# Kernel optimization log

Hardware: AMD Instinct MI355X
Metric: run time of the kernel (lower is better)

Reference implementation:

```python
import jax, jax.numpy as jnp
import numpy as np

N, E, D, H, HID = 50000, 400000, 64, 8, 1024
NEG_SLOPE = 0.2
BN_EPS = 1e-5


def setup_inputs() -> dict:
    key = jax.random.key(0)
    ks = jax.random.split(key, 10)
    s = 0.05
    return {
        "x": jax.random.normal(ks[0], (N, D), jnp.float32),
        "src": jax.random.randint(ks[1], (E,), 0, N, jnp.int32),
        "dst": jax.random.randint(ks[2], (E,), 0, N, jnp.int32),
        "fc_w": jax.random.normal(ks[3], (H * D, D), jnp.float32) * s,
        "attn_l": jax.random.normal(ks[4], (H, D), jnp.float32) * s,
        "attn_r": jax.random.normal(ks[5], (H, D), jnp.float32) * s,
        "gat_bias": jnp.zeros((H * D,), jnp.float32),
        "bn1_gamma": jnp.ones((H * D,), jnp.float32),
        "bn1_beta": jnp.zeros((H * D,), jnp.float32),
        "w1": jax.random.normal(ks[6], (HID, H * D), jnp.float32) * s,
        "b1": jnp.zeros((HID,), jnp.float32),
        "w2": jax.random.normal(ks[7], (D, HID), jnp.float32) * s,
        "b2": jnp.zeros((D,), jnp.float32),
        "bn2_gamma": jnp.ones((D,), jnp.float32),
        "bn2_beta": jnp.zeros((D,), jnp.float32),
    }


def _batchnorm(h, gamma, beta):
    # training-mode BatchNorm1d: batch statistics over node axis
    mu = h.mean(axis=0)
    var = h.var(axis=0)
    return gamma * (h - mu) * jax.lax.rsqrt(var + BN_EPS) + beta


def reference(x, src, dst, fc_w, attn_l, attn_r, gat_bias,
              bn1_gamma, bn1_beta, w1, b1, w2, b2, bn2_gamma, bn2_beta):
    n = x.shape[0]
    nh, dh = attn_l.shape
    # --- GATConv ---
    feat = (x @ fc_w.T).reshape(n, nh, dh)                 # [N,H,Dh]
    el = jnp.einsum("nhd,hd->nh", feat, attn_l)            # [N,H]
    er = jnp.einsum("nhd,hd->nh", feat, attn_r)            # [N,H]
    e = jax.nn.leaky_relu(el[src] + er[dst], NEG_SLOPE)    # [E,H]
    # edge softmax grouped by destination node (numerically stable)
    emax = jax.ops.segment_max(e, dst, num_segments=n)
    emax = jnp.where(jnp.isfinite(emax), emax, 0.0)        # nodes w/ no in-edges
    ez = jnp.exp(e - emax[dst])
    denom = jax.ops.segment_sum(ez, dst, num_segments=n)
    alpha = ez / denom[dst]                                # [E,H]
    msg = alpha[:, :, None] * feat[src]                    # [E,H,Dh]
    rst = jax.ops.segment_sum(msg, dst, num_segments=n)    # [N,H,Dh]
    rst = rst + gat_bias.reshape(nh, dh)
    h = rst.reshape(n, nh * dh)                            # flatten(1)
    # --- feed forward: BN -> Linear -> ReLU -> Linear -> BN ---
    h = _batchnorm(h, bn1_gamma, bn1_beta)
    h = jax.nn.relu(h @ w1.T + b1)
    h = h @ w2.T + b2
    h = _batchnorm(h, bn2_gamma, bn2_beta)
    return h
```

## Files before the change

kernel.cpp:

```cpp
#include <hip/hip_runtime.h>

#define NEG_SLOPE 0.2f
#define BN_EPS 1e-5f

typedef __bf16 bf16x8 __attribute__((ext_vector_type(8)));
typedef float  f32x4  __attribute__((ext_vector_type(4)));
typedef unsigned short ushort8_t __attribute__((ext_vector_type(8)));

__device__ __forceinline__ unsigned short f2bf(float f) {
    unsigned int u = __float_as_uint(f);
    unsigned int r = u + 0x7FFFu + ((u >> 16) & 1u);
    return (unsigned short)(r >> 16);
}
__device__ __forceinline__ float bf2f(unsigned short u) {
    return __uint_as_float(((unsigned int)u) << 16);
}
__device__ __forceinline__ void gload16(const void* g, void* l) {
    __builtin_amdgcn_global_load_lds(
        (const __attribute__((address_space(1))) unsigned int*)g,
        (__attribute__((address_space(3))) unsigned int*)l, 16, 0, 0);
}

__global__ __launch_bounds__(256)
void prep(const float* __restrict__ x, const int* __restrict__ dst,
          const float* __restrict__ fc_w, const float* __restrict__ w2,
          const float* __restrict__ attn_l, const float* __restrict__ attn_r,
          unsigned short* __restrict__ xbf, unsigned short* __restrict__ fcwbf,
          unsigned short* __restrict__ w2bf, float* __restrict__ proj,
          int* __restrict__ counts, int totX4, int E,
          int bCvtx, int bHist, int bFcw, int bW2)
{
    const int bid = blockIdx.x, tid = threadIdx.x;
    if (bid < bCvtx) {
        int i4 = bid * 256 + tid;
        if (i4 < totX4) {
            float4 v = *(const float4*)(x + (size_t)i4 * 4);
            ushort4 o = {f2bf(v.x), f2bf(v.y), f2bf(v.z), f2bf(v.w)};
            *(ushort4*)(xbf + (size_t)i4 * 4) = o;
        }
    } else if (bid < bHist) {
        int base = (bid - bCvtx) * 1024 + tid;
        #pragma unroll
        for (int k = 0; k < 4; ++k) {
            int e = base + k * 256;
            if (e < E) atomicAdd(&counts[dst[e]], 1);
        }
    } else if (bid < bFcw) {
        int i4 = (bid - bHist) * 256 + tid;
        if (i4 < 8192) {
            float4 v = *(const float4*)(fc_w + (size_t)i4 * 4);
            ushort4 o = {f2bf(v.x), f2bf(v.y), f2bf(v.z), f2bf(v.w)};
            *(ushort4*)(fcwbf + (size_t)i4 * 4) = o;
        }
    } else if (bid < bW2) {
        int i4 = (bid - bFcw) * 256 + tid;
        if (i4 < 16384) {
            float4 v = *(const float4*)(w2 + (size_t)i4 * 4);
            ushort4 o = {f2bf(v.x), f2bf(v.y), f2bf(v.z), f2bf(v.w)};
            *(ushort4*)(w2bf + (size_t)i4 * 4) = o;
        }
    } else {
        for (int t2 = tid; t2 < 512; t2 += 256) {
            int h = t2 >> 6, k = t2 & 63;
            float al = 0.f, ar = 0.f;
            for (int d = 0; d < 64; ++d) {
                float w = fc_w[(size_t)(h * 64 + d) * 64 + k];
                al = fmaf(attn_l[h * 64 + d], w, al);
                ar = fmaf(attn_r[h * 64 + d], w, ar);
            }
            proj[t2] = al;
            proj[512 + t2] = ar;
        }
    }
}

__global__ __launch_bounds__(256)
void scan1_elr(const int* __restrict__ counts, int* __restrict__ incl,
               int* __restrict__ bsum, int N, int NB,
               const float* __restrict__ x, const float* __restrict__ proj,
               float* __restrict__ el, float* __restrict__ er, int NH)
{
    __shared__ int sm[256];
    if ((int)blockIdx.x < NB) {
        int i = blockIdx.x * 256 + threadIdx.x;
        int v = (i < N) ? counts[i] : 0;
        sm[threadIdx.x] = v;
        __syncthreads();
        #pragma unroll
        for (int d = 1; d < 256; d <<= 1) {
            int t = (threadIdx.x >= d) ? sm[threadIdx.x - d] : 0;
            __syncthreads();
            sm[threadIdx.x] += t;
            __syncthreads();
        }
        if (i < N) incl[i] = sm[threadIdx.x];
        if (threadIdx.x == 255) bsum[blockIdx.x] = sm[255];
    } else {
        int idx = (blockIdx.x - NB) * 256 + threadIdx.x;
        if (idx >= NH) return;
        int h = idx & 7, n = idx >> 3;
        const float4* f  = (const float4*)(x + (size_t)n * 64);
        const float4* pl = (const float4*)(proj + h * 64);
        const float4* pr = (const float4*)(proj + 512 + h * 64);
        float sl = 0.f, sr = 0.f;
        #pragma unroll
        for (int i = 0; i < 16; ++i) {
            float4 fv = f[i], lv = pl[i], rv = pr[i];
            sl += fv.x * lv.x + fv.y * lv.y + fv.z * lv.z + fv.w * lv.w;
            sr += fv.x * rv.x + fv.y * rv.y + fv.z * rv.z + fv.w * rv.w;
        }
        el[idx] = sl;
        er[idx] = sr;
    }
}

__global__ void scan2(int* __restrict__ bsum, int nb) {
    __shared__ int sm[256];
    int v = (threadIdx.x < nb) ? bsum[threadIdx.x] : 0;
    sm[threadIdx.x] = v;
    __syncthreads();
    #pragma unroll
    for (int d = 1; d < 256; d <<= 1) {
        int t = (threadIdx.x >= d) ? sm[threadIdx.x - d] : 0;
        __syncthreads();
        sm[threadIdx.x] += t;
        __syncthreads();
    }
    if (threadIdx.x < nb) bsum[threadIdx.x] = sm[threadIdx.x] - v;
}
__global__ void scan3(const int* __restrict__ incl, const int* __restrict__ bsum,
                      int* __restrict__ row_ptr, int* __restrict__ cursor, int N) {
    int i = blockIdx.x * 256 + threadIdx.x;
    if (i < N) {
        int v = incl[i] + bsum[blockIdx.x];
        row_ptr[i + 1] = v;
        cursor[i + 1] = v;
    }
    if (i == 0) { row_ptr[0] = 0; cursor[0] = 0; }
}
__global__ void scatter_edges(const int* __restrict__ src, const int* __restrict__ dst,
                              int* __restrict__ cursor, int* __restrict__ esrc, int E) {
    int e = blockIdx.x * 256 + threadIdx.x;
    if (e < E) {
        int p = atomicAdd(&cursor[dst[e]], 1);
        esrc[p] = src[e];
    }
}

__global__ __launch_bounds__(256)
void gat_aggregate(const int* __restrict__ row_ptr, const int* __restrict__ esrc,
                   const float* __restrict__ el, const float* __restrict__ er,
                   const unsigned short* __restrict__ xb, unsigned short* __restrict__ xagg,
                   int N)
{
    int node = blockIdx.x * 4 + (threadIdx.x >> 6);
    if (node >= N) return;
    const int lane = threadIdx.x & 63;
    const int h = lane >> 3, j = lane & 7;
    const int beg = row_ptr[node], end = row_ptr[node + 1];
    const float er_n = er[node * 8 + h];

    float denom = 0.f;
    float a[8] = {};
    for (int k = beg; k < end; ++k) {
        int s = esrc[k];
        float v = el[s * 8 + h] + er_n;
        v = (v > 0.f) ? v : NEG_SLOPE * v;
        float z = __expf(v);
        denom += z;
        ushort8_t fv = *(const ushort8_t*)(xb + (size_t)s * 64 + j * 8);
        #pragma unroll
        for (int t = 0; t < 8; ++t) a[t] = fmaf(z, bf2f(fv[t]), a[t]);
    }
    float inv = (end > beg) ? 1.f / denom : 0.f;
    ushort8_t o;
    #pragma unroll
    for (int t = 0; t < 8; ++t) o[t] = f2bf(a[t] * inv);
    *(ushort8_t*)(xagg + (size_t)node * 512 + lane * 8) = o;
}

__global__ __launch_bounds__(256)
void head_transform(const unsigned short* __restrict__ Xa,
                    const unsigned short* __restrict__ Fw,
                    const float* __restrict__ gat_bias,
                    unsigned short* __restrict__ H,
                    float* __restrict__ sums1, int M)
{
    __shared__ alignas(16) char Asm[128 * 64 * 2];
    __shared__ alignas(16) char Bsm[64 * 64 * 2];
    __shared__ float reds[4][64], redq[4][64];
    const int tid = threadIdx.x, lane = tid & 63, wave = tid >> 6;
    const int bm = blockIdx.x * 128;
    const int head = blockIdx.y;
    const int lr = lane >> 3, lk = ((lane & 7) ^ lr) * 8;

    #pragma unroll
    for (int it = 0; it < 4; ++it) {
        int seg = wave * 4 + it;
        gload16(Xa + (size_t)(bm + seg * 8 + lr) * 512 + head * 64 + lk, Asm + seg * 1024);
    }
    #pragma unroll
    for (int it = 0; it < 2; ++it) {
        int seg = wave * 2 + it;
        gload16(Fw + (size_t)(head * 64 + seg * 8 + lr) * 64 + lk, Bsm + seg * 1024);
    }
    __syncthreads();

    f32x4 acc[2][4] = {};
    #pragma unroll
    for (int kk = 0; kk < 2; ++kk) {
        int kg = kk * 4 + (lane >> 4);
        bf16x8 a[2], b[4];
        #pragma unroll
        for (int i = 0; i < 2; ++i) {
            int row = wave * 32 + i * 16 + (lane & 15);
            a[i] = *(const bf16x8*)(Asm + row * 128 + ((kg ^ (row & 7)) << 4));
        }
        #pragma unroll
        for (int j = 0; j < 4; ++j) {
            int row = j * 16 + (lane & 15);
            b[j] = *(const bf16x8*)(Bsm + row * 128 + ((kg ^ (row & 7)) << 4));
        }
        #pragma unroll
        for (int i = 0; i < 2; ++i)
            #pragma unroll
            for (int j = 0; j < 4; ++j)
                acc[i][j] = __builtin_amdgcn_mfma_f32_16x16x32_bf16(a[i], b[j], acc[i][j], 0, 0, 0);
    }

    float s4[4] = {}, q4[4] = {};
    #pragma unroll
    for (int j = 0; j < 4; ++j) {
        int col = j * 16 + (lane & 15);
        float bias = gat_bias[head * 64 + col];
        #pragma unroll
        for (int i = 0; i < 2; ++i)
            #pragma unroll
            for (int r = 0; r < 4; ++r) {
                int gm = bm + wave * 32 + i * 16 + (lane >> 4) * 4 + r;
                if (gm < M) {
                    unsigned short hb = f2bf(acc[i][j][r] + bias);
                    H[(size_t)gm * 512 + head * 64 + col] = hb;
                    float vq = bf2f(hb);
                    s4[j] += vq; q4[j] += vq * vq;
                }
            }
    }
    #pragma unroll
    for (int j = 0; j < 4; ++j) {
        s4[j] += __shfl_xor(s4[j], 16); q4[j] += __shfl_xor(q4[j], 16);
        s4[j] += __shfl_xor(s4[j], 32); q4[j] += __shfl_xor(q4[j], 32);
    }
    if (lane < 16) {
        #pragma unroll
        for (int j = 0; j < 4; ++j) {
            reds[wave][j * 16 + lane] = s4[j];
            redq[wave][j * 16 + lane] = q4[j];
        }
    }
    __syncthreads();
    if (wave == 0 && lane < 16) {
        #pragma unroll
        for (int j = 0; j < 4; ++j) {
            int c = j * 16 + lane;
            atomicAdd(&sums1[head * 64 + c], reds[0][c] + reds[1][c] + reds[2][c] + reds[3][c]);
            atomicAdd(&sums1[512 + head * 64 + c], redq[0][c] + redq[1][c] + redq[2][c] + redq[3][c]);
        }
    }
}

__global__ __launch_bounds__(256)
void fold_w1(const float* __restrict__ w1, const float* __restrict__ sums1,
             const float* __restrict__ gamma, const float* __restrict__ beta,
             const float* __restrict__ b1, unsigned short* __restrict__ w1p,
             float* __restrict__ b1p, float invM)
{
    __shared__ float sa[512], sb[512];
    for (int c = threadIdx.x; c < 512; c += 256) {
        float mu = sums1[c] * invM;
        float var = sums1[512 + c] * invM - mu * mu;
        float a = gamma[c] * rsqrtf(var + BN_EPS);
        sa[c] = a;
        sb[c] = beta[c] - a * mu;
    }
    __syncthreads();
    int n = blockIdx.x * 4 + (threadIdx.x >> 6);
    int lane = threadIdx.x & 63;
    const float* wrow = w1 + (size_t)n * 512 + lane * 8;
    float p = 0.f;
    ushort8_t o;
    #pragma unroll
    for (int t = 0; t < 8; ++t) {
        float w = wrow[t];
        o[t] = f2bf(w * sa[lane * 8 + t]);
        p = fmaf(w, sb[lane * 8 + t], p);
    }
    *(ushort8_t*)(w1p + (size_t)n * 512 + lane * 8) = o;
    #pragma unroll
    for (int d = 1; d < 64; d <<= 1) p += __shfl_xor(p, d);
    if (lane == 0) b1p[n] = b1[n] + p;
}

__global__ __launch_bounds__(256)
void gemm2p(const unsigned short* __restrict__ A,
            const unsigned short* __restrict__ B,
            const unsigned short* __restrict__ W2,
            const float* __restrict__ b1p,
            unsigned short* __restrict__ P, int M)
{
    __shared__ alignas(16) char smem[49152];
    char* Abuf0 = smem;
    char* Abuf1 = smem + 16384;
    char* Bbuf  = smem + 32768;
    char* TR   = smem;
    char* Wbuf = smem + 32768;
    char* PK   = smem + 32768;

    const int tid = threadIdx.x, lane = tid & 63, wave = tid >> 6;
    const int wr = wave >> 1, wc = wave & 1;
    const int lr = lane >> 3, lk = ((lane & 7) ^ lr) * 8;

    int bid = blockIdx.x;
    int wgid = (bid & 7) * 391 + (bid >> 3);
    const int bm = (wgid >> 3) * 128;
    const int t  = wgid & 7;
    const int bn = t * 128;

    #pragma unroll
    for (int it = 0; it < 4; ++it) {
        int seg = wave * 4 + it;
        gload16(A + (size_t)(bm + seg * 8 + lr) * 512 + lk, Abuf0 + seg * 1024);
    }

    f32x4 acc[4][4] = {};
    #pragma unroll
    for (int ks = 0; ks < 8; ++ks) {
        const int k0 = ks * 64;
        #pragma unroll
        for (int it = 0; it < 4; ++it) {
            int seg = wave * 4 + it;
            gload16(B + (size_t)(bn + seg * 8 + lr) * 512 + k0 + lk, Bbuf + seg * 1024);
        }
        if (ks < 7) {
            char* An = (ks & 1) ? Abuf0 : Abuf1;
            #pragma unroll
            for (int it = 0; it < 4; ++it) {
                int seg = wave * 4 + it;
                gload16(A + (size_t)(bm + seg * 8 + lr) * 512 + (k0 + 64) + lk, An + seg * 1024);
            }
            asm volatile("s_waitcnt vmcnt(4)" ::: "memory");
        } else {
            asm volatile("s_waitcnt vmcnt(0)" ::: "memory");
        }
        __builtin_amdgcn_s_barrier();
        __builtin_amdgcn_sched_barrier(0);
        const char* Ac = (ks & 1) ? Abuf1 : Abuf0;
        #pragma unroll
        for (int kk = 0; kk < 2; ++kk) {
            int kg = kk * 4 + (lane >> 4);
            bf16x8 a[4], b[4];
            #pragma unroll
            for (int i = 0; i < 4; ++i) {
                int row = wr * 64 + i * 16 + (lane & 15);
                a[i] = *(const bf16x8*)(Ac + row * 128 + ((kg ^ (row & 7)) << 4));
            }
            #pragma unroll
            for (int j = 0; j < 4; ++j) {
                int row = wc * 64 + j * 16 + (lane & 15);
                b[j] = *(const bf16x8*)(Bbuf + row * 128 + ((kg ^ (row & 7)) << 4));
            }
            #pragma unroll
            for (int i = 0; i < 4; ++i)
                #pragma unroll
                for (int j = 0; j < 4; ++j)
                    acc[i][j] = __builtin_amdgcn_mfma_f32_16x16x32_bf16(a[i], b[j], acc[i][j], 0, 0, 0);
        }
        __builtin_amdgcn_sched_barrier(0);
        __builtin_amdgcn_s_barrier();
        __builtin_amdgcn_sched_barrier(0);
    }

    #pragma unroll
    for (int j = 0; j < 4; ++j) {
        int c = wc * 64 + j * 16 + (lane & 15);
        float bs = b1p[bn + c];
        #pragma unroll
        for (int i = 0; i < 4; ++i)
            #pragma unroll
            for (int r = 0; r < 4; ++r) {
                int rw = wr * 64 + i * 16 + (lane >> 4) * 4 + r;
                float v = fmaxf(acc[i][j][r] + bs, 0.f);
                *(unsigned short*)(TR + rw * 256 + (((c >> 3) ^ (rw & 7)) << 4) + (c & 7) * 2) = f2bf(v);
            }
    }
    #pragma unroll
    for (int it = 0; it < 4; ++it) {
        int oc = wave * 16 + it * 4 + (lane >> 4);
        int g = lane & 15;
        gload16(W2 + (size_t)oc * 1024 + bn + ((g ^ (oc & 7))) * 8, Wbuf + (wave * 4 + it) * 1024);
    }
    __syncthreads();

    f32x4 pacc[2][4] = {};
    #pragma unroll
    for (int ks = 0; ks < 4; ++ks) {
        int kg2 = ks * 4 + (lane >> 4);
        #pragma unroll
        for (int i = 0; i < 2; ++i) {
            int arow = wave * 32 + i * 16 + (lane & 15);
            bf16x8 av = *(const bf16x8*)(TR + arow * 256 + ((kg2 ^ (arow & 7)) << 4));
            #pragma unroll
            for (int j = 0; j < 4; ++j) {
                int oc = j * 16 + (lane & 15);
                bf16x8 bv = *(const bf16x8*)(Wbuf + oc * 256 + ((kg2 ^ (oc & 7)) << 4));
                pacc[i][j] = __builtin_amdgcn_mfma_f32_16x16x32_bf16(av, bv, pacc[i][j], 0, 0, 0);
            }
        }
    }
    __syncthreads();

    #pragma unroll
    for (int i = 0; i < 2; ++i)
        #pragma unroll
        for (int j = 0; j < 4; ++j)
            #pragma unroll
            for (int r = 0; r < 4; ++r) {
                int row = wave * 32 + i * 16 + (lane >> 4) * 4 + r;
                int col = j * 16 + (lane & 15);
                *(unsigned short*)(PK + row * 128 + col * 2) = f2bf(pacc[i][j][r]);
            }
    __syncthreads();
    unsigned short* Pt = P + (size_t)t * M * 64;
    #pragma unroll
    for (int it = 0; it < 4; ++it) {
        int u = it * 256 + tid;
        int row = u >> 3, g8 = u & 7;
        int gm = bm + row;
        if (gm < M) {
            uint4 v = *(const uint4*)(PK + row * 128 + g8 * 16);
            *(uint4*)(Pt + (size_t)gm * 64 + g8 * 8) = v;
        }
    }
}

__global__ __launch_bounds__(256)
void reduce_bn2(const unsigned short* __restrict__ P, const float* __restrict__ b2,
                float* __restrict__ out, int M, float* __restrict__ sums2)
{
    __shared__ float ls[256], lq[256];
    int c = threadIdx.x & 63, g = threadIdx.x >> 6;
    const size_t S = (size_t)M * 64;
    float bias = b2[c];
    float s = 0.f, q = 0.f;
    for (int r = blockIdx.x * 4 + g; r < M; r += gridDim.x * 4) {
        size_t idx = (size_t)r * 64 + c;
        float v = bias;
        #pragma unroll
        for (int t = 0; t < 8; ++t) v += bf2f(P[t * S + idx]);
        out[idx] = v;
        s += v; q += v * v;
    }
    ls[threadIdx.x] = s; lq[threadIdx.x] = q;
    __syncthreads();
    if (g == 0) {
        s = ls[c] + ls[64 + c] + ls[128 + c] + ls[192 + c];
        q = lq[c] + lq[64 + c] + lq[128 + c] + lq[192 + c];
        atomicAdd(&sums2[c], s);
        atomicAdd(&sums2[64 + c], q);
    }
}

__global__ __launch_bounds__(256)
void bn_apply64(float* __restrict__ X, const float* __restrict__ sums2,
                const float* __restrict__ gamma, const float* __restrict__ beta,
                int M, float invM)
{
    int c = threadIdx.x & 63, g = threadIdx.x >> 6;
    float mu = sums2[c] * invM;
    float var = sums2[64 + c] * invM - mu * mu;
    float a = gamma[c] * rsqrtf(var + BN_EPS);
    float b = beta[c] - a * mu;
    for (int r = blockIdx.x * 4 + g; r < M; r += gridDim.x * 4) {
        size_t i = (size_t)r * 64 + c;
        X[i] = fmaf(a, X[i], b);
    }
}

extern "C" void kernel_launch(void* const* d_in, const int* in_sizes, int n_in,
                              void* d_out, int out_size, void* d_ws, size_t ws_size,
                              hipStream_t stream)
{
    const float* x         = (const float*)d_in[0];
    const int*   src       = (const int*)d_in[1];
    const int*   dst       = (const int*)d_in[2];
    const float* fc_w      = (const float*)d_in[3];
    const float* attn_l    = (const float*)d_in[4];
    const float* attn_r    = (const float*)d_in[5];
    const float* gat_bias  = (const float*)d_in[6];
    const float* bn1_gamma = (const float*)d_in[7];
    const float* bn1_beta  = (const float*)d_in[8];
    const float* w1        = (const float*)d_in[9];
    const float* b1        = (const float*)d_in[10];
    const float* w2        = (const float*)d_in[11];
    const float* b2        = (const float*)d_in[12];
    const float* bn2_gamma = (const float*)d_in[13];
    const float* bn2_beta  = (const float*)d_in[14];
    float* out = (float*)d_out;

    const int D = 64, HD = 512, HID = 1024;
    const int N = in_sizes[0] / D;
    const int E = in_sizes[1];
    const int NH = N * 8;
    const int NB = (N + 255) / 256;
    const int Mpad = ((N + 127) / 128) * 128 + 128;

    size_t off = 0;
    auto alloc = [&](size_t bytes) -> void* {
        void* p = (char*)d_ws + off;
        off += (bytes + 255) & ~(size_t)255;
        return p;
    };
    void* regionA = alloc((size_t)Mpad * HD * 2);
    unsigned short* xagg = (unsigned short*)regionA;
    unsigned short* P    = (unsigned short*)regionA;
    unsigned short* hbf  = (unsigned short*)alloc((size_t)Mpad * HD * 2);
    unsigned short* xbf  = (unsigned short*)alloc((size_t)N * D * 2);
    unsigned short* fcwbf = (unsigned short*)alloc((size_t)HD * D * 2);
    unsigned short* w1p  = (unsigned short*)alloc((size_t)HID * HD * 2);
    unsigned short* w2bf = (unsigned short*)alloc((size_t)D * HID * 2);
    float* b1p   = (float*)alloc(HID * 4);
    float* proj  = (float*)alloc(2 * 512 * 4);
    float* el    = (float*)alloc((size_t)NH * 4);
    float* er    = (float*)alloc((size_t)NH * 4);
    char* zbase  = (char*)d_ws + off;
    int* counts  = (int*)alloc((size_t)N * 4);
    float* sums1 = (float*)alloc(2 * 512 * 4);
    float* sums2 = (float*)alloc(2 * 64 * 4);
    size_t zbytes = ((char*)d_ws + off) - zbase;
    int* incl    = (int*)alloc((size_t)N * 4);
    int* row_ptr = (int*)alloc((size_t)(N + 1) * 4);
    int* cursor  = (int*)alloc((size_t)(N + 1) * 4);
    int* bsum    = (int*)alloc(256 * 4);
    int* esrc    = (int*)alloc((size_t)E * 4);
    (void)ws_size; (void)n_in; (void)out_size;

    hipMemsetAsync(zbase, 0, zbytes, stream);

    {
        int totX4 = (N * D) / 4;
        int bCvtx = (totX4 + 255) / 256;
        int bHist = bCvtx + (E + 1023) / 1024;
        int bFcw  = bHist + 32;
        int bW2   = bFcw + 64;
        int grid  = bW2 + 1;
        prep<<<grid, 256, 0, stream>>>(x, dst, fc_w, w2, attn_l, attn_r,
                                       xbf, fcwbf, w2bf, proj, counts,
                                       totX4, E, bCvtx, bHist, bFcw, bW2);
    }

    scan1_elr<<<NB + (NH + 255) / 256, 256, 0, stream>>>(counts, incl, bsum, N, NB,
                                                         x, proj, el, er, NH);
    scan2<<<1, 256, 0, stream>>>(bsum, NB);
    scan3<<<NB, 256, 0, stream>>>(incl, bsum, row_ptr, cursor, N);
    scatter_edges<<<(E + 255) / 256, 256, 0, stream>>>(src, dst, cursor, esrc, E);

    gat_aggregate<<<(N + 3) / 4, 256, 0, stream>>>(row_ptr, esrc, el, er, xbf, xagg, N);

    {
        dim3 grid((N + 127) / 128, 8);
        head_transform<<<grid, 256, 0, stream>>>(xagg, fcwbf, gat_bias, hbf, sums1, N);
    }
    fold_w1<<<HID / 4, 256, 0, stream>>>(w1, sums1, bn1_gamma, bn1_beta, b1, w1p, b1p, 1.f / N);

    {
        int nwg = ((N + 127) / 128) * 8;
        gemm2p<<<nwg, 256, 0, stream>>>(hbf, w1p, w2bf, b1p, P, N);
    }

    reduce_bn2<<<1024, 256, 0, stream>>>(P, b2, out, N, sums2);
    bn_apply64<<<1024, 256, 0, stream>>>(out, sums2, bn2_gamma, bn2_beta, N, 1.f / N);
}
```

Baseline: 293.0 us.

## Fold fc_w and BN1 into W1, drop materialized H, atomically accumulate output

```diff
diff --git a/kernel.cpp b/kernel.cpp
--- a/kernel.cpp
+++ b/kernel.cpp
@@ -25,10 +25,12 @@
 void prep(const float* __restrict__ x, const int* __restrict__ dst,
           const float* __restrict__ fc_w, const float* __restrict__ w2,
           const float* __restrict__ attn_l, const float* __restrict__ attn_r,
+          const float* __restrict__ b2,
           unsigned short* __restrict__ xbf, unsigned short* __restrict__ fcwbf,
           unsigned short* __restrict__ w2bf, float* __restrict__ proj,
-          int* __restrict__ counts, int totX4, int E,
-          int bCvtx, int bHist, int bFcw, int bW2)
+          int* __restrict__ counts, float* __restrict__ outp,
+          int totX4, int E, int totO4,
+          int bCvtx, int bHist, int bFcw, int bW2, int bOut)
 {
     const int bid = blockIdx.x, tid = threadIdx.x;
     if (bid < bCvtx) {
@@ -58,6 +60,12 @@
             float4 v = *(const float4*)(w2 + (size_t)i4 * 4);
             ushort4 o = {f2bf(v.x), f2bf(v.y), f2bf(v.z), f2bf(v.w)};
             *(ushort4*)(w2bf + (size_t)i4 * 4) = o;
+        }
+    } else if (bid < bOut) {
+        int i4 = (bid - bW2) * 256 + tid;
+        if (i4 < totO4) {
+            float4 v = *(const float4*)(b2 + (i4 & 15) * 4);
+            *(float4*)(outp + (size_t)i4 * 4) = v;
         }
     } else {
         for (int t2 = tid; t2 < 512; t2 += 256) {
@@ -114,30 +122,28 @@
     }
 }
 
-__global__ void scan2(int* __restrict__ bsum, int nb) {
+__global__ void scan23(const int* __restrict__ incl, const int* __restrict__ bsum,
+                       int* __restrict__ row_ptr, int* __restrict__ cursor, int N, int NB)
+{
     __shared__ int sm[256];
-    int v = (threadIdx.x < nb) ? bsum[threadIdx.x] : 0;
-    sm[threadIdx.x] = v;
+    int t = threadIdx.x;
+    sm[t] = (t < (int)blockIdx.x && t < NB) ? bsum[t] : 0;
     __syncthreads();
     #pragma unroll
-    for (int d = 1; d < 256; d <<= 1) {
-        int t = (threadIdx.x >= d) ? sm[threadIdx.x - d] : 0;
+    for (int d = 128; d > 0; d >>= 1) {
+        if (t < d) sm[t] += sm[t + d];
         __syncthreads();
-        sm[threadIdx.x] += t;
-        __syncthreads();
-    }
-    if (threadIdx.x < nb) bsum[threadIdx.x] = sm[threadIdx.x] - v;
-}
-__global__ void scan3(const int* __restrict__ incl, const int* __restrict__ bsum,
-                      int* __restrict__ row_ptr, int* __restrict__ cursor, int N) {
-    int i = blockIdx.x * 256 + threadIdx.x;
+    }
+    int pre = sm[0];
+    int i = blockIdx.x * 256 + t;
     if (i < N) {
-        int v = incl[i] + bsum[blockIdx.x];
+        int v = incl[i] + pre;
         row_ptr[i + 1] = v;
         cursor[i + 1] = v;
     }
     if (i == 0) { row_ptr[0] = 0; cursor[0] = 0; }
 }
+
 __global__ void scatter_edges(const int* __restrict__ src, const int* __restrict__ dst,
                               int* __restrict__ cursor, int* __restrict__ esrc, int E) {
     int e = blockIdx.x * 256 + threadIdx.x;
@@ -162,15 +168,18 @@
 
     float denom = 0.f;
     float a[8] = {};
+    int s_cur = (beg < end) ? esrc[beg] : 0;
     for (int k = beg; k < end; ++k) {
-        int s = esrc[k];
-        float v = el[s * 8 + h] + er_n;
+        int s_nxt = (k + 1 < end) ? esrc[k + 1] : 0;
+        float elv = el[s_cur * 8 + h];
+        ushort8_t fv = *(const ushort8_t*)(xb + (size_t)s_cur * 64 + j * 8);
+        float v = elv + er_n;
         v = (v > 0.f) ? v : NEG_SLOPE * v;
         float z = __expf(v);
         denom += z;
-        ushort8_t fv = *(const ushort8_t*)(xb + (size_t)s * 64 + j * 8);
         #pragma unroll
         for (int t = 0; t < 8; ++t) a[t] = fmaf(z, bf2f(fv[t]), a[t]);
+        s_cur = s_nxt;
     }
     float inv = (end > beg) ? 1.f / denom : 0.f;
     ushort8_t o;
@@ -180,11 +189,10 @@
 }
 
 __global__ __launch_bounds__(256)
-void head_transform(const unsigned short* __restrict__ Xa,
-                    const unsigned short* __restrict__ Fw,
-                    const float* __restrict__ gat_bias,
-                    unsigned short* __restrict__ H,
-                    float* __restrict__ sums1, int M)
+void bn1_stats(const unsigned short* __restrict__ Xa,
+               const unsigned short* __restrict__ Fw,
+               const float* __restrict__ gat_bias,
+               float* __restrict__ sums1, int M)
 {
     __shared__ alignas(16) char Asm[128 * 64 * 2];
     __shared__ alignas(16) char Bsm[64 * 64 * 2];
@@ -239,9 +247,7 @@
             for (int r = 0; r < 4; ++r) {
                 int gm = bm + wave * 32 + i * 16 + (lane >> 4) * 4 + r;
                 if (gm < M) {
-                    unsigned short hb = f2bf(acc[i][j][r] + bias);
-                    H[(size_t)gm * 512 + head * 64 + col] = hb;
-                    float vq = bf2f(hb);
+                    float vq = bf2f(f2bf(acc[i][j][r] + bias));
                     s4[j] += vq; q4[j] += vq * vq;
                 }
             }
@@ -270,35 +276,72 @@
 }
 
 __global__ __launch_bounds__(256)
-void fold_w1(const float* __restrict__ w1, const float* __restrict__ sums1,
-             const float* __restrict__ gamma, const float* __restrict__ beta,
-             const float* __restrict__ b1, unsigned short* __restrict__ w1p,
-             float* __restrict__ b1p, float invM)
-{
-    __shared__ float sa[512], sb[512];
-    for (int c = threadIdx.x; c < 512; c += 256) {
-        float mu = sums1[c] * invM;
-        float var = sums1[512 + c] * invM - mu * mu;
-        float a = gamma[c] * rsqrtf(var + BN_EPS);
-        sa[c] = a;
-        sb[c] = beta[c] - a * mu;
-    }
-    __syncthreads();
-    int n = blockIdx.x * 4 + (threadIdx.x >> 6);
-    int lane = threadIdx.x & 63;
-    const float* wrow = w1 + (size_t)n * 512 + lane * 8;
-    float p = 0.f;
-    ushort8_t o;
-    #pragma unroll
-    for (int t = 0; t < 8; ++t) {
-        float w = wrow[t];
-        o[t] = f2bf(w * sa[lane * 8 + t]);
-        p = fmaf(w, sb[lane * 8 + t], p);
-    }
-    *(ushort8_t*)(w1p + (size_t)n * 512 + lane * 8) = o;
-    #pragma unroll
-    for (int d = 1; d < 64; d <<= 1) p += __shfl_xor(p, d);
-    if (lane == 0) b1p[n] = b1[n] + p;
+void fold(const float* __restrict__ w1, const float* __restrict__ fc_w,
+          const float* __restrict__ sums1, const float* __restrict__ gamma,
+          const float* __restrict__ beta, const float* __restrict__ gat_bias,
+          const float* __restrict__ b1, unsigned short* __restrict__ wtil,
+          float* __restrict__ b1p, float invM)
+{
+    const int bid = blockIdx.x, tid = threadIdx.x;
+    if (bid < 64) {
+        __shared__ float sF[64][65];
+        __shared__ float sa[64];
+        int ot = bid >> 3, h = bid & 7;
+        if (tid < 64) {
+            int c = h * 64 + tid;
+            float mu = sums1[c] * invM;
+            float var = sums1[512 + c] * invM - mu * mu;
+            sa[tid] = gamma[c] * rsqrtf(var + BN_EPS);
+        }
+        for (int e = 0; e < 16; ++e) {
+            int idx = tid * 16 + e;
+            int d = idx >> 6, k = idx & 63;
+            sF[k][d] = fc_w[(size_t)(h * 64 + d) * 64 + k];
+        }
+        __syncthreads();
+        int ol = tid >> 1, half = tid & 1;
+        int o = ot * 128 + ol;
+        int kbase = half * 32;
+        float acc[32];
+        #pragma unroll
+        for (int i = 0; i < 32; ++i) acc[i] = 0.f;
+        const float* wrow = w1 + (size_t)o * 512 + h * 64;
+        #pragma unroll
+        for (int dc = 0; dc < 4; ++dc) {
+            float wa[16];
+            #pragma unroll
+            for (int d = 0; d < 16; ++d) wa[d] = wrow[dc * 16 + d] * sa[dc * 16 + d];
+            #pragma unroll
+            for (int kk2 = 0; kk2 < 32; ++kk2) {
+                float s = acc[kk2];
+                #pragma unroll
+                for (int d = 0; d < 16; ++d) s = fmaf(wa[d], sF[kbase + kk2][dc * 16 + d], s);
+                acc[kk2] = s;
+            }
+        }
+        unsigned int* orow = (unsigned int*)(wtil + (size_t)o * 512 + h * 64 + kbase);
+        #pragma unroll
+        for (int i = 0; i < 16; ++i)
+            orow[i] = (unsigned int)f2bf(acc[2 * i]) | ((unsigned int)f2bf(acc[2 * i + 1]) << 16);
+    } else {
+        __shared__ float ss[512];
+        for (int c = tid; c < 512; c += 256) {
+            float mu = sums1[c] * invM;
+            float var = sums1[512 + c] * invM - mu * mu;
+            float a = gamma[c] * rsqrtf(var + BN_EPS);
+            ss[c] = beta[c] + a * (gat_bias[c] - mu);
+        }
+        __syncthreads();
+        int wave = tid >> 6, lane = tid & 63;
+        int o = (bid - 64) * 4 + wave;
+        const float* wrow = w1 + (size_t)o * 512 + lane * 8;
+        float p = 0.f;
+        #pragma unroll
+        for (int t2 = 0; t2 < 8; ++t2) p = fmaf(wrow[t2], ss[lane * 8 + t2], p);
+        #pragma unroll
+        for (int d = 1; d < 64; d <<= 1) p += __shfl_xor(p, d);
+        if (lane == 0) b1p[o] = b1[o] + p;
+    }
 }
 
 __global__ __launch_bounds__(256)
@@ -306,7 +349,8 @@
             const unsigned short* __restrict__ B,
             const unsigned short* __restrict__ W2,
             const float* __restrict__ b1p,
-            unsigned short* __restrict__ P, int M)
+            float* __restrict__ outp,
+            int M)
 {
     __shared__ alignas(16) char smem[49152];
     char* Abuf0 = smem;
@@ -314,7 +358,6 @@
     char* Bbuf  = smem + 32768;
     char* TR   = smem;
     char* Wbuf = smem + 32768;
-    char* PK   = smem + 32768;
 
     const int tid = threadIdx.x, lane = tid & 63, wave = tid >> 6;
     const int wr = wave >> 1, wc = wave & 1;
@@ -417,7 +460,6 @@
             }
         }
     }
-    __syncthreads();
 
     #pragma unroll
     for (int i = 0; i < 2; ++i)
@@ -425,39 +467,20 @@
         for (int j = 0; j < 4; ++j)
             #pragma unroll
             for (int r = 0; r < 4; ++r) {
-                int row = wave * 32 + i * 16 + (lane >> 4) * 4 + r;
+                int gm = bm + wave * 32 + i * 16 + (lane >> 4) * 4 + r;
                 int col = j * 16 + (lane & 15);
-                *(unsigned short*)(PK + row * 128 + col * 2) = f2bf(pacc[i][j][r]);
-            }
-    __syncthreads();
-    unsigned short* Pt = P + (size_t)t * M * 64;
-    #pragma unroll
-    for (int it = 0; it < 4; ++it) {
-        int u = it * 256 + tid;
-        int row = u >> 3, g8 = u & 7;
-        int gm = bm + row;
-        if (gm < M) {
-            uint4 v = *(const uint4*)(PK + row * 128 + g8 * 16);
-            *(uint4*)(Pt + (size_t)gm * 64 + g8 * 8) = v;
-        }
-    }
-}
-
-__global__ __launch_bounds__(256)
-void reduce_bn2(const unsigned short* __restrict__ P, const float* __restrict__ b2,
-                float* __restrict__ out, int M, float* __restrict__ sums2)
+                if (gm < M) atomicAdd(&outp[(size_t)gm * 64 + col], pacc[i][j][r]);
+            }
+}
+
+__global__ __launch_bounds__(256)
+void bn2_stats(const float* __restrict__ outp, int M, float* __restrict__ sums2)
 {
     __shared__ float ls[256], lq[256];
     int c = threadIdx.x & 63, g = threadIdx.x >> 6;
-    const size_t S = (size_t)M * 64;
-    float bias = b2[c];
     float s = 0.f, q = 0.f;
     for (int r = blockIdx.x * 4 + g; r < M; r += gridDim.x * 4) {
-        size_t idx = (size_t)r * 64 + c;
-        float v = bias;
-        #pragma unroll
-        for (int t = 0; t < 8; ++t) v += bf2f(P[t * S + idx]);
-        out[idx] = v;
+        float v = outp[(size_t)r * 64 + c];
         s += v; q += v * v;
     }
     ls[threadIdx.x] = s; lq[threadIdx.x] = q;
@@ -520,13 +543,10 @@
         off += (bytes + 255) & ~(size_t)255;
         return p;
     };
-    void* regionA = alloc((size_t)Mpad * HD * 2);
-    unsigned short* xagg = (unsigned short*)regionA;
-    unsigned short* P    = (unsigned short*)regionA;
-    unsigned short* hbf  = (unsigned short*)alloc((size_t)Mpad * HD * 2);
+    unsigned short* xagg = (unsigned short*)alloc((size_t)Mpad * HD * 2);
     unsigned short* xbf  = (unsigned short*)alloc((size_t)N * D * 2);
     unsigned short* fcwbf = (unsigned short*)alloc((size_t)HD * D * 2);
-    unsigned short* w1p  = (unsigned short*)alloc((size_t)HID * HD * 2);
+    unsigned short* wtil = (unsigned short*)alloc((size_t)HID * HD * 2);
     unsigned short* w2bf = (unsigned short*)alloc((size_t)D * HID * 2);
     float* b1p   = (float*)alloc(HID * 4);
     float* proj  = (float*)alloc(2 * 512 * 4);
@@ -548,35 +568,37 @@
 
     {
         int totX4 = (N * D) / 4;
+        int totO4 = (N * D) / 4;
         int bCvtx = (totX4 + 255) / 256;
         int bHist = bCvtx + (E + 1023) / 1024;
         int bFcw  = bHist + 32;
         int bW2   = bFcw + 64;
-        int grid  = bW2 + 1;
-        prep<<<grid, 256, 0, stream>>>(x, dst, fc_w, w2, attn_l, attn_r,
-                                       xbf, fcwbf, w2bf, proj, counts,
-                                       totX4, E, bCvtx, bHist, bFcw, bW2);
+        int bOut  = bW2 + (totO4 + 255) / 256;
+        int grid  = bOut + 1;
+        prep<<<grid, 256, 0, stream>>>(x, dst, fc_w, w2, attn_l, attn_r, b2,
+                                       xbf, fcwbf, w2bf, proj, counts, out,
+                                       totX4, E, totO4, bCvtx, bHist, bFcw, bW2, bOut);
     }
 
     scan1_elr<<<NB + (NH + 255) / 256, 256, 0, stream>>>(counts, incl, bsum, N, NB,
                                                          x, proj, el, er, NH);
-    scan2<<<1, 256, 0, stream>>>(bsum, NB);
-    scan3<<<NB, 256, 0, stream>>>(incl, bsum, row_ptr, cursor, N);
+    scan23<<<NB, 256, 0, stream>>>(incl, bsum, row_ptr, cursor, N, NB);
     scatter_edges<<<(E + 255) / 256, 256, 0, stream>>>(src, dst, cursor, esrc, E);
 
     gat_aggregate<<<(N + 3) / 4, 256, 0, stream>>>(row_ptr, esrc, el, er, xbf, xagg, N);
 
     {
         dim3 grid((N + 127) / 128, 8);
-        head_transform<<<grid, 256, 0, stream>>>(xagg, fcwbf, gat_bias, hbf, sums1, N);
-    }
-    fold_w1<<<HID / 4, 256, 0, stream>>>(w1, sums1, bn1_gamma, bn1_beta, b1, w1p, b1p, 1.f / N);
+        bn1_stats<<<grid, 256, 0, stream>>>(xagg, fcwbf, gat_bias, sums1, N);
+    }
+    fold<<<320, 256, 0, stream>>>(w1, fc_w, sums1, bn1_gamma, bn1_beta, gat_bias,
+                                  b1, wtil, b1p, 1.f / N);
 
     {
         int nwg = ((N + 127) / 128) * 8;
-        gemm2p<<<nwg, 256, 0, stream>>>(hbf, w1p, w2bf, b1p, P, N);
-    }
-
-    reduce_bn2<<<1024, 256, 0, stream>>>(P, b2, out, N, sums2);
+        gemm2p<<<nwg, 256, 0, stream>>>(xagg, wtil, w2bf, b1p, out, N);
+    }
+
+    bn2_stats<<<1024, 256, 0, stream>>>(out, N, sums2);
     bn_apply64<<<1024, 256, 0, stream>>>(out, sums2, bn2_gamma, bn2_beta, N, 1.f / N);
 }
```

Measured after the change: 332.4 us. 1.13x slower.
